# Optimization experiments

Measured on AMD Instinct MI355X. Metric: run time of the kernel, lower is better.

Reference implementation:

```python
import jax, jax.numpy as jnp
import numpy as np

SIGMA = 0.4            # gaussian geodesic kernel width (class default)
B, N_IN, N_OUT, C, K = 2, 163842, 40962, 128, 7  # icosphere rank 7 -> rank 6, valence-7 candidates


def setup_inputs() -> dict:
    key = jax.random.key(0)
    k_x, k_p, k_o, k_c, k_d = jax.random.split(key, 5)
    x = jax.random.normal(k_x, (B, N_IN, C), dtype=jnp.float32)
    parent_idx = jax.random.randint(k_p, (N_IN,), 0, N_OUT)
    omega = jax.random.uniform(k_o, (N_IN,), dtype=jnp.float32, minval=0.5, maxval=1.5)
    omega = omega / omega.mean()          # matches omega / omega.mean() in __init__
    cand_idx = jax.random.randint(k_c, (N_IN, K), 0, N_OUT)
    cand_mask = jnp.ones((N_IN, K), dtype=jnp.float32)
    delta = jax.random.uniform(k_d, (N_IN, K), dtype=jnp.float32, minval=0.0, maxval=0.5)
    return dict(x=x, omega=omega, delta=delta, cand_mask=cand_mask,
                parent_idx=parent_idx, cand_idx=cand_idx)


def reference(x, omega, delta, cand_mask, parent_idx, cand_idx):
    # --- AreaWeightedDownsample: weight, scatter-add to coarse nodes, normalize ---
    weighted = x * omega[None, :, None]                        # [B, N_in, C]
    down = jnp.zeros((x.shape[0], N_OUT, x.shape[2]), x.dtype)
    down = down.at[:, parent_idx].add(weighted)                # scatter_add over node dim
    denom = jnp.zeros((N_OUT,), x.dtype).at[parent_idx].add(omega)
    down = down / jnp.clip(denom, 1e-8)[None, :, None]         # [B, N_out, C]
    # --- GeodesicKernelUpsample: gather K coarse candidates, gaussian geodesic weights ---
    w = jnp.exp(-(delta * delta) / (2.0 * SIGMA * SIGMA)) * cand_mask   # [N_in, K]
    w = w / jnp.clip(w.sum(axis=-1, keepdims=True), 1e-8)
    gathered = down[:, cand_idx]                               # [B, N_in, K, C]
    return jnp.einsum('nk,bnkc->bnc', w, gathered)             # [B, N_in, C]
```

## Files before the change

kernel.cpp:

```cpp
#include <hip/hip_runtime.h>
#include <hip/hip_bf16.h>

#define B_SZ   2
#define N_IN   163842
#define N_OUT  40962
#define C_DIM  128
#define K_CAND 7
#define INV_2SIG2 3.125f

#define SCAN_T 1024
#define NBLK_SCAN ((N_OUT + SCAN_T - 1) / SCAN_T)

typedef float f32x4 __attribute__((ext_vector_type(4)));
typedef unsigned short u16x8 __attribute__((ext_vector_type(8)));

__device__ __forceinline__ float bf2f(unsigned short u) {
    return __uint_as_float((unsigned)u << 16);
}
__device__ __forceinline__ unsigned short f2bf(float f) {
    unsigned u = __float_as_uint(f);
    return (unsigned short)((u + 0x7fffu + ((u >> 16) & 1u)) >> 16);
}

__global__ __launch_bounds__(256) void count_kernel(
    const int* __restrict__ parent, int* __restrict__ count)
{
    int n = blockIdx.x * 256 + threadIdx.x;
    if (n < N_IN) atomicAdd(&count[parent[n]], 1);
}

__global__ __launch_bounds__(SCAN_T) void scan1_kernel(
    const int* __restrict__ count, int* __restrict__ offs, int* __restrict__ bsum)
{
    __shared__ int wsum[SCAN_T / 64];
    const int t    = threadIdx.x;
    const int lane = t & 63;
    const int wid  = t >> 6;
    const int j    = blockIdx.x * SCAN_T + t;
    const int c = (j < N_OUT) ? count[j] : 0;

    int v = c;
    #pragma unroll
    for (int off = 1; off < 64; off <<= 1) {
        int u = __shfl_up(v, off, 64);
        if (lane >= off) v += u;
    }
    if (lane == 63) wsum[wid] = v;
    __syncthreads();
    if (wid == 0 && lane < SCAN_T / 64) {
        int w = wsum[lane];
        #pragma unroll
        for (int off = 1; off < SCAN_T / 64; off <<= 1) {
            int u = __shfl_up(w, off, 64);
            if (lane >= off) w += u;
        }
        wsum[lane] = w;
    }
    __syncthreads();
    const int wbase = (wid == 0) ? 0 : wsum[wid - 1];
    if (j < N_OUT) offs[j] = wbase + v - c;
    if (t == 0) bsum[blockIdx.x] = wsum[SCAN_T / 64 - 1];
}

__global__ __launch_bounds__(64) void scan2_kernel(
    const int* __restrict__ bsum, int* __restrict__ bbase)
{
    const int lane = threadIdx.x;
    int s = (lane < NBLK_SCAN) ? bsum[lane] : 0;
    int v = s;
    #pragma unroll
    for (int off = 1; off < 64; off <<= 1) {
        int u = __shfl_up(v, off, 64);
        if (lane >= off) v += u;
    }
    if (lane < NBLK_SCAN) bbase[lane] = v - s;
}

__global__ __launch_bounds__(SCAN_T) void scan3_kernel(
    int* __restrict__ offs, const int* __restrict__ bbase)
{
    const int j = blockIdx.x * SCAN_T + threadIdx.x;
    if (j < N_OUT && blockIdx.x > 0) offs[j] += bbase[blockIdx.x];
}

__global__ __launch_bounds__(256) void fill_kernel(
    const int* __restrict__ parent, const int* __restrict__ offs,
    const float* __restrict__ omega,
    int* __restrict__ count, int* __restrict__ perm,
    float* __restrict__ om_perm)
{
    int n = blockIdx.x * 256 + threadIdx.x;
    if (n < N_IN) {
        const int p = parent[n];
        const float om = omega[n];
        const int pos = offs[p] + atomicSub(&count[p], 1) - 1;
        perm[pos] = n;
        om_perm[pos] = om;
    }
}

__global__ __launch_bounds__(256) void reduce_kernel(
    const float* __restrict__ x,
    const int*   __restrict__ offs,
    const int*   __restrict__ perm,
    const float* __restrict__ om_perm,
    __hip_bfloat16* __restrict__ down)
{
    const int wid  = threadIdx.x >> 6;
    const int lane = threadIdx.x & 63;
    const int p = blockIdx.x * 4 + wid;
    if (p >= N_OUT) return;

    const int beg = offs[p];
    const int end = (p + 1 < N_OUT) ? offs[p + 1] : N_IN;
    const int cnt = end - beg;

    const int half = lane >> 5;
    const int l    = lane & 31;
    const f32x4* x4 = (const f32x4*)x;
    const size_t bofs = (size_t)half * N_IN * 32;

    f32x4 acc = {0.f, 0.f, 0.f, 0.f};
    float ds = 0.f;

    for (int cbase = 0; cbase < cnt; cbase += 64) {
        const int m = min(64, cnt - cbase);
        int   myn  = 0;
        float myom = 0.f;
        if (lane < m) {
            myn  = perm[beg + cbase + lane];
            myom = om_perm[beg + cbase + lane];
        }
        #pragma unroll 4
        for (int j = 0; j < m; ++j) {
            const int   n  = __shfl(myn,  j);
            const float om = __shfl(myom, j);
            ds += om;
            const f32x4 v = __builtin_nontemporal_load(&x4[bofs + (size_t)n * 32 + l]);
            acc.x = fmaf(v.x, om, acc.x);
            acc.y = fmaf(v.y, om, acc.y);
            acc.z = fmaf(v.z, om, acc.z);
            acc.w = fmaf(v.w, om, acc.w);
        }
    }
    const float inv = 1.f / fmaxf(ds, 1e-8f);

    ushort4 hh;
    hh.x = f2bf(acc.x * inv);
    hh.y = f2bf(acc.y * inv);
    hh.z = f2bf(acc.z * inv);
    hh.w = f2bf(acc.w * inv);
    ((ushort4*)down)[((size_t)half * N_OUT + p) * 32 + l] = hh;
}

__global__ __launch_bounds__(256) void gather_kernel(
    const float* __restrict__ delta,
    const float* __restrict__ cand_mask,
    const int*   __restrict__ cand_idx,
    const __hip_bfloat16* __restrict__ down,
    float* __restrict__ out)
{
    const int wid  = threadIdx.x >> 6;
    const int lane = threadIdx.x & 63;
    const int grp  = lane >> 5;
    const int l5   = lane & 31;
    const int n0   = blockIdx.x * 16 + wid * 4 + grp * 2;
    if (n0 >= N_IN) return;
    const bool r1ok = (n0 + 1 < N_IN);

    const int sub = l5 >> 3;
    const int ls  = l5 & 7;
    float w = 0.f;
    int pidx = 0;
    if (sub < 2 && ls < K_CAND && (sub == 0 || r1ok)) {
        const int n = n0 + sub;
        const float d   = delta[(size_t)n * K_CAND + ls];
        const float msk = cand_mask[(size_t)n * K_CAND + ls];
        pidx = cand_idx[(size_t)n * K_CAND + ls];
        w = __expf(-d * d * INV_2SIG2) * msk;
    }
    float s = w;
    s += __shfl_xor(s, 1, 8);
    s += __shfl_xor(s, 2, 8);
    s += __shfl_xor(s, 4, 8);
    const float coef = w / fmaxf(s, 1e-8f);

    float cf[2][K_CAND];
    int   pk[2][K_CAND];
    #pragma unroll
    for (int r = 0; r < 2; ++r) {
        #pragma unroll
        for (int k = 0; k < K_CAND; ++k) {
            cf[r][k] = __shfl(coef, r * 8 + k, 32);
            pk[r][k] = __shfl(pidx, r * 8 + k, 32);
        }
    }

    const int half = l5 >> 4;
    const int l4   = l5 & 15;
    const u16x8* d8 = (const u16x8*)down;
    const size_t bofs = (size_t)half * N_OUT * 16;

    u16x8 v[2][K_CAND];
    #pragma unroll
    for (int r = 0; r < 2; ++r)
        #pragma unroll
        for (int k = 0; k < K_CAND; ++k)
            v[r][k] = d8[bofs + (size_t)pk[r][k] * 16 + l4];

    f32x4* o4 = (f32x4*)out;
    #pragma unroll
    for (int r = 0; r < 2; ++r) {
        f32x4 acc0 = {0.f, 0.f, 0.f, 0.f};
        f32x4 acc1 = {0.f, 0.f, 0.f, 0.f};
        #pragma unroll
        for (int k = 0; k < K_CAND; ++k) {
            const float c = cf[r][k];
            acc0.x = fmaf(c, bf2f(v[r][k].s0), acc0.x);
            acc0.y = fmaf(c, bf2f(v[r][k].s1), acc0.y);
            acc0.z = fmaf(c, bf2f(v[r][k].s2), acc0.z);
            acc0.w = fmaf(c, bf2f(v[r][k].s3), acc0.w);
            acc1.x = fmaf(c, bf2f(v[r][k].s4), acc1.x);
            acc1.y = fmaf(c, bf2f(v[r][k].s5), acc1.y);
            acc1.z = fmaf(c, bf2f(v[r][k].s6), acc1.z);
            acc1.w = fmaf(c, bf2f(v[r][k].s7), acc1.w);
        }
        if (r == 0 || r1ok) {
            const size_t obase = ((size_t)half * N_IN + n0 + r) * 32 + (size_t)l4 * 2;
            __builtin_nontemporal_store(acc0, &o4[obase]);
            __builtin_nontemporal_store(acc1, &o4[obase + 1]);
        }
    }
}

extern "C" void kernel_launch(void* const* d_in, const int* in_sizes, int n_in,
                              void* d_out, int out_size, void* d_ws, size_t ws_size,
                              hipStream_t stream) {
    const float* x         = (const float*)d_in[0];
    const float* omega     = (const float*)d_in[1];
    const float* delta     = (const float*)d_in[2];
    const float* cand_mask = (const float*)d_in[3];
    const int*   parent    = (const int*)d_in[4];
    const int*   cand_idx  = (const int*)d_in[5];
    float* out = (float*)d_out;

    __hip_bfloat16* down = (__hip_bfloat16*)d_ws;
    int*   count   = (int*)(down + (size_t)B_SZ * N_OUT * C_DIM);
    int*   offs    = count + N_OUT;
    int*   perm    = offs + N_OUT;
    float* om_perm = (float*)(perm + N_IN);
    int*   bsum    = (int*)(om_perm + N_IN);
    int*   bbase   = bsum + NBLK_SCAN;

    hipMemsetAsync(count, 0, (size_t)N_OUT * sizeof(int), stream);

    const int nblk = (N_IN + 255) / 256;
    count_kernel<<<nblk, 256, 0, stream>>>(parent, count);
    scan1_kernel<<<NBLK_SCAN, SCAN_T, 0, stream>>>(count, offs, bsum);
    scan2_kernel<<<1, 64, 0, stream>>>(bsum, bbase);
    scan3_kernel<<<NBLK_SCAN, SCAN_T, 0, stream>>>(offs, bbase);
    fill_kernel<<<nblk, 256, 0, stream>>>(parent, offs, omega, count, perm, om_perm);
    reduce_kernel<<<(N_OUT + 3) / 4, 256, 0, stream>>>(x, offs, perm, om_perm, down);
    gather_kernel<<<(N_IN + 15) / 16, 256, 0, stream>>>(
        delta, cand_mask, cand_idx, down, out);
}
```

Baseline: 397.1 us.

## Persistent grid-stride gather with metadata prefetch and interleaved batch layout for down

The gather kernel becomes persistent with a fixed grid. It prefetches the next pair's delta, mask and index loads while the current pair's candidate rows are gathered and accumulated. The down buffer is stored with both batches interleaved per coarse node, so each candidate fetch reads one contiguous 512-byte row instead of two separate rows. The reduce unroll and launch bounds are also raised. The intent is to hide index-load latency and improve gather locality, at the cost of higher register pressure and a fixed grid size.

```diff
diff --git a/kernel.cpp b/kernel.cpp
--- a/kernel.cpp
+++ b/kernel.cpp
@@ -10,6 +10,7 @@
 
 #define SCAN_T 1024
 #define NBLK_SCAN ((N_OUT + SCAN_T - 1) / SCAN_T)
+#define GATHER_BLOCKS 2048
 
 typedef float f32x4 __attribute__((ext_vector_type(4)));
 typedef unsigned short u16x8 __attribute__((ext_vector_type(8)));
@@ -99,7 +100,7 @@
     }
 }
 
-__global__ __launch_bounds__(256) void reduce_kernel(
+__global__ __launch_bounds__(256, 4) void reduce_kernel(
     const float* __restrict__ x,
     const int*   __restrict__ offs,
     const int*   __restrict__ perm,
@@ -131,7 +132,7 @@
             myn  = perm[beg + cbase + lane];
             myom = om_perm[beg + cbase + lane];
         }
-        #pragma unroll 4
+        #pragma unroll 8
         for (int j = 0; j < m; ++j) {
             const int   n  = __shfl(myn,  j);
             const float om = __shfl(myom, j);
@@ -150,10 +151,10 @@
     hh.y = f2bf(acc.y * inv);
     hh.z = f2bf(acc.z * inv);
     hh.w = f2bf(acc.w * inv);
-    ((ushort4*)down)[((size_t)half * N_OUT + p) * 32 + l] = hh;
-}
-
-__global__ __launch_bounds__(256) void gather_kernel(
+    ((ushort4*)down)[(size_t)p * 64 + lane] = hh;
+}
+
+__global__ __launch_bounds__(256, 4) void gather_kernel(
     const float* __restrict__ delta,
     const float* __restrict__ cand_mask,
     const int*   __restrict__ cand_idx,
@@ -164,72 +165,90 @@
     const int lane = threadIdx.x & 63;
     const int grp  = lane >> 5;
     const int l5   = lane & 31;
-    const int n0   = blockIdx.x * 16 + wid * 4 + grp * 2;
-    if (n0 >= N_IN) return;
-    const bool r1ok = (n0 + 1 < N_IN);
+    const int gid  = (blockIdx.x * 4 + wid) * 2 + grp;
+    const int ngroups = GATHER_BLOCKS * 8;
+    const int npairs  = N_IN / 2;
 
     const int sub = l5 >> 3;
     const int ls  = l5 & 7;
+
+    const u16x8* d8 = (const u16x8*)down;
+    f32x4* o4 = (f32x4*)out;
+    const int half = l5 >> 4;
+    const int c16  = l5 & 15;
+
     float w = 0.f;
     int pidx = 0;
-    if (sub < 2 && ls < K_CAND && (sub == 0 || r1ok)) {
-        const int n = n0 + sub;
-        const float d   = delta[(size_t)n * K_CAND + ls];
-        const float msk = cand_mask[(size_t)n * K_CAND + ls];
-        pidx = cand_idx[(size_t)n * K_CAND + ls];
-        w = __expf(-d * d * INV_2SIG2) * msk;
-    }
-    float s = w;
-    s += __shfl_xor(s, 1, 8);
-    s += __shfl_xor(s, 2, 8);
-    s += __shfl_xor(s, 4, 8);
-    const float coef = w / fmaxf(s, 1e-8f);
-
-    float cf[2][K_CAND];
-    int   pk[2][K_CAND];
-    #pragma unroll
-    for (int r = 0; r < 2; ++r) {
-        #pragma unroll
-        for (int k = 0; k < K_CAND; ++k) {
-            cf[r][k] = __shfl(coef, r * 8 + k, 32);
-            pk[r][k] = __shfl(pidx, r * 8 + k, 32);
-        }
-    }
-
-    const int half = l5 >> 4;
-    const int l4   = l5 & 15;
-    const u16x8* d8 = (const u16x8*)down;
-    const size_t bofs = (size_t)half * N_OUT * 16;
-
-    u16x8 v[2][K_CAND];
-    #pragma unroll
-    for (int r = 0; r < 2; ++r)
-        #pragma unroll
-        for (int k = 0; k < K_CAND; ++k)
-            v[r][k] = d8[bofs + (size_t)pk[r][k] * 16 + l4];
-
-    f32x4* o4 = (f32x4*)out;
-    #pragma unroll
-    for (int r = 0; r < 2; ++r) {
-        f32x4 acc0 = {0.f, 0.f, 0.f, 0.f};
-        f32x4 acc1 = {0.f, 0.f, 0.f, 0.f};
-        #pragma unroll
-        for (int k = 0; k < K_CAND; ++k) {
-            const float c = cf[r][k];
-            acc0.x = fmaf(c, bf2f(v[r][k].s0), acc0.x);
-            acc0.y = fmaf(c, bf2f(v[r][k].s1), acc0.y);
-            acc0.z = fmaf(c, bf2f(v[r][k].s2), acc0.z);
-            acc0.w = fmaf(c, bf2f(v[r][k].s3), acc0.w);
-            acc1.x = fmaf(c, bf2f(v[r][k].s4), acc1.x);
-            acc1.y = fmaf(c, bf2f(v[r][k].s5), acc1.y);
-            acc1.z = fmaf(c, bf2f(v[r][k].s6), acc1.z);
-            acc1.w = fmaf(c, bf2f(v[r][k].s7), acc1.w);
-        }
-        if (r == 0 || r1ok) {
-            const size_t obase = ((size_t)half * N_IN + n0 + r) * 32 + (size_t)l4 * 2;
+    {
+        const int pi = gid;
+        if (pi < npairs && sub < 2 && ls < K_CAND) {
+            const int n = pi * 2 + sub;
+            const float d   = __builtin_nontemporal_load(&delta[(size_t)n * K_CAND + ls]);
+            const float msk = __builtin_nontemporal_load(&cand_mask[(size_t)n * K_CAND + ls]);
+            pidx = __builtin_nontemporal_load(&cand_idx[(size_t)n * K_CAND + ls]);
+            w = __expf(-d * d * INV_2SIG2) * msk;
+        }
+    }
+
+    for (int pi = gid; pi < npairs; pi += ngroups) {
+        float s = w;
+        s += __shfl_xor(s, 1, 8);
+        s += __shfl_xor(s, 2, 8);
+        s += __shfl_xor(s, 4, 8);
+        const float coef = w / fmaxf(s, 1e-8f);
+
+        float cf[2][K_CAND];
+        int   pk[2][K_CAND];
+        #pragma unroll
+        for (int r = 0; r < 2; ++r)
+            #pragma unroll
+            for (int k = 0; k < K_CAND; ++k) {
+                cf[r][k] = __shfl(coef, r * 8 + k, 32);
+                pk[r][k] = __shfl(pidx, r * 8 + k, 32);
+            }
+
+        u16x8 v[2][K_CAND];
+        #pragma unroll
+        for (int r = 0; r < 2; ++r)
+            #pragma unroll
+            for (int k = 0; k < K_CAND; ++k)
+                v[r][k] = d8[(size_t)pk[r][k] * 32 + l5];
+
+        const int pn = pi + ngroups;
+        float w2 = 0.f;
+        int pidx2 = 0;
+        if (pn < npairs && sub < 2 && ls < K_CAND) {
+            const int n = pn * 2 + sub;
+            const float d   = __builtin_nontemporal_load(&delta[(size_t)n * K_CAND + ls]);
+            const float msk = __builtin_nontemporal_load(&cand_mask[(size_t)n * K_CAND + ls]);
+            pidx2 = __builtin_nontemporal_load(&cand_idx[(size_t)n * K_CAND + ls]);
+            w2 = __expf(-d * d * INV_2SIG2) * msk;
+        }
+
+        const int n0 = pi * 2;
+        #pragma unroll
+        for (int r = 0; r < 2; ++r) {
+            f32x4 acc0 = {0.f, 0.f, 0.f, 0.f};
+            f32x4 acc1 = {0.f, 0.f, 0.f, 0.f};
+            #pragma unroll
+            for (int k = 0; k < K_CAND; ++k) {
+                const float c = cf[r][k];
+                acc0.x = fmaf(c, bf2f(v[r][k].s0), acc0.x);
+                acc0.y = fmaf(c, bf2f(v[r][k].s1), acc0.y);
+                acc0.z = fmaf(c, bf2f(v[r][k].s2), acc0.z);
+                acc0.w = fmaf(c, bf2f(v[r][k].s3), acc0.w);
+                acc1.x = fmaf(c, bf2f(v[r][k].s4), acc1.x);
+                acc1.y = fmaf(c, bf2f(v[r][k].s5), acc1.y);
+                acc1.z = fmaf(c, bf2f(v[r][k].s6), acc1.z);
+                acc1.w = fmaf(c, bf2f(v[r][k].s7), acc1.w);
+            }
+            const size_t obase = ((size_t)half * N_IN + n0 + r) * 32 + (size_t)c16 * 2;
             __builtin_nontemporal_store(acc0, &o4[obase]);
             __builtin_nontemporal_store(acc1, &o4[obase + 1]);
         }
+
+        w = w2;
+        pidx = pidx2;
     }
 }
 
@@ -261,6 +280,6 @@
     scan3_kernel<<<NBLK_SCAN, SCAN_T, 0, stream>>>(offs, bbase);
     fill_kernel<<<nblk, 256, 0, stream>>>(parent, offs, omega, count, perm, om_perm);
     reduce_kernel<<<(N_OUT + 3) / 4, 256, 0, stream>>>(x, offs, perm, om_perm, down);
-    gather_kernel<<<(N_IN + 15) / 16, 256, 0, stream>>>(
+    gather_kernel<<<GATHER_BLOCKS, 256, 0, stream>>>(
         delta, cand_mask, cand_idx, down, out);
 }
```

After: 404.1 us. Within noise of the previous version (+1.8%).

## Interleave batch dimension in bf16 coarse buffer so each gather reads contiguous 256B rows

Applied to the files above, without the earlier changes.

The coarse bf16 buffer moves from [B][N_out][C] to [N_out][B][C], so both batch rows of a coarse node sit next to each other. The reduce kernel now has each half-wave handle one coarse node for both batches, and the gather kernel has each half-wave handle one fine node and fetch one contiguous 512B row per candidate. The aim is to halve the index and weight loads per batch and improve locality of the random gather. In exchange each lane issues fewer independent loads per thread in the gather (7 instead of 14), which may reduce memory-level parallelism.

```diff
diff --git a/kernel.cpp b/kernel.cpp
--- a/kernel.cpp
+++ b/kernel.cpp
@@ -108,49 +108,55 @@
 {
     const int wid  = threadIdx.x >> 6;
     const int lane = threadIdx.x & 63;
-    const int p = blockIdx.x * 4 + wid;
+    const int grp  = lane >> 5;
+    const int l5   = lane & 31;
+    const int p = blockIdx.x * 8 + wid * 2 + grp;
     if (p >= N_OUT) return;
 
     const int beg = offs[p];
     const int end = (p + 1 < N_OUT) ? offs[p + 1] : N_IN;
     const int cnt = end - beg;
 
-    const int half = lane >> 5;
-    const int l    = lane & 31;
     const f32x4* x4 = (const f32x4*)x;
-    const size_t bofs = (size_t)half * N_IN * 32;
-
-    f32x4 acc = {0.f, 0.f, 0.f, 0.f};
+
+    f32x4 acc0 = {0.f, 0.f, 0.f, 0.f};
+    f32x4 acc1 = {0.f, 0.f, 0.f, 0.f};
     float ds = 0.f;
 
-    for (int cbase = 0; cbase < cnt; cbase += 64) {
-        const int m = min(64, cnt - cbase);
+    for (int cbase = 0; cbase < cnt; cbase += 32) {
+        const int m = min(32, cnt - cbase);
         int   myn  = 0;
         float myom = 0.f;
-        if (lane < m) {
-            myn  = perm[beg + cbase + lane];
-            myom = om_perm[beg + cbase + lane];
+        if (l5 < m) {
+            myn  = perm[beg + cbase + l5];
+            myom = om_perm[beg + cbase + l5];
         }
         #pragma unroll 4
         for (int j = 0; j < m; ++j) {
-            const int   n  = __shfl(myn,  j);
-            const float om = __shfl(myom, j);
+            const int   n  = __shfl(myn,  j, 32);
+            const float om = __shfl(myom, j, 32);
             ds += om;
-            const f32x4 v = __builtin_nontemporal_load(&x4[bofs + (size_t)n * 32 + l]);
-            acc.x = fmaf(v.x, om, acc.x);
-            acc.y = fmaf(v.y, om, acc.y);
-            acc.z = fmaf(v.z, om, acc.z);
-            acc.w = fmaf(v.w, om, acc.w);
+            const f32x4 v0 = __builtin_nontemporal_load(&x4[(size_t)n * 32 + l5]);
+            const f32x4 v1 = __builtin_nontemporal_load(&x4[((size_t)N_IN + n) * 32 + l5]);
+            acc0.x = fmaf(v0.x, om, acc0.x);
+            acc0.y = fmaf(v0.y, om, acc0.y);
+            acc0.z = fmaf(v0.z, om, acc0.z);
+            acc0.w = fmaf(v0.w, om, acc0.w);
+            acc1.x = fmaf(v1.x, om, acc1.x);
+            acc1.y = fmaf(v1.y, om, acc1.y);
+            acc1.z = fmaf(v1.z, om, acc1.z);
+            acc1.w = fmaf(v1.w, om, acc1.w);
         }
     }
     const float inv = 1.f / fmaxf(ds, 1e-8f);
 
-    ushort4 hh;
-    hh.x = f2bf(acc.x * inv);
-    hh.y = f2bf(acc.y * inv);
-    hh.z = f2bf(acc.z * inv);
-    hh.w = f2bf(acc.w * inv);
-    ((ushort4*)down)[((size_t)half * N_OUT + p) * 32 + l] = hh;
+    ushort4 h0, h1;
+    h0.x = f2bf(acc0.x * inv); h0.y = f2bf(acc0.y * inv);
+    h0.z = f2bf(acc0.z * inv); h0.w = f2bf(acc0.w * inv);
+    h1.x = f2bf(acc1.x * inv); h1.y = f2bf(acc1.y * inv);
+    h1.z = f2bf(acc1.z * inv); h1.w = f2bf(acc1.w * inv);
+    ((ushort4*)down)[(size_t)p * 64 + l5]      = h0;
+    ((ushort4*)down)[(size_t)p * 64 + 32 + l5] = h1;
 }
 
 __global__ __launch_bounds__(256) void gather_kernel(
@@ -164,19 +170,15 @@
     const int lane = threadIdx.x & 63;
     const int grp  = lane >> 5;
     const int l5   = lane & 31;
-    const int n0   = blockIdx.x * 16 + wid * 4 + grp * 2;
-    if (n0 >= N_IN) return;
-    const bool r1ok = (n0 + 1 < N_IN);
-
-    const int sub = l5 >> 3;
-    const int ls  = l5 & 7;
+    const int n    = blockIdx.x * 8 + wid * 2 + grp;
+    if (n >= N_IN) return;
+
     float w = 0.f;
     int pidx = 0;
-    if (sub < 2 && ls < K_CAND && (sub == 0 || r1ok)) {
-        const int n = n0 + sub;
-        const float d   = delta[(size_t)n * K_CAND + ls];
-        const float msk = cand_mask[(size_t)n * K_CAND + ls];
-        pidx = cand_idx[(size_t)n * K_CAND + ls];
+    if (l5 < K_CAND) {
+        const float d   = __builtin_nontemporal_load(&delta[(size_t)n * K_CAND + l5]);
+        const float msk = __builtin_nontemporal_load(&cand_mask[(size_t)n * K_CAND + l5]);
+        pidx = __builtin_nontemporal_load(&cand_idx[(size_t)n * K_CAND + l5]);
         w = __expf(-d * d * INV_2SIG2) * msk;
     }
     float s = w;
@@ -185,52 +187,40 @@
     s += __shfl_xor(s, 4, 8);
     const float coef = w / fmaxf(s, 1e-8f);
 
-    float cf[2][K_CAND];
-    int   pk[2][K_CAND];
-    #pragma unroll
-    for (int r = 0; r < 2; ++r) {
-        #pragma unroll
-        for (int k = 0; k < K_CAND; ++k) {
-            cf[r][k] = __shfl(coef, r * 8 + k, 32);
-            pk[r][k] = __shfl(pidx, r * 8 + k, 32);
-        }
-    }
-
+    float cf[K_CAND];
+    int   pk[K_CAND];
+    #pragma unroll
+    for (int k = 0; k < K_CAND; ++k) {
+        cf[k] = __shfl(coef, k, 32);
+        pk[k] = __shfl(pidx, k, 32);
+    }
+
+    const u16x8* d8 = (const u16x8*)down;
+    u16x8 v[K_CAND];
+    #pragma unroll
+    for (int k = 0; k < K_CAND; ++k)
+        v[k] = d8[(size_t)pk[k] * 32 + l5];
+
+    f32x4 acc0 = {0.f, 0.f, 0.f, 0.f};
+    f32x4 acc1 = {0.f, 0.f, 0.f, 0.f};
+    #pragma unroll
+    for (int k = 0; k < K_CAND; ++k) {
+        const float c = cf[k];
+        acc0.x = fmaf(c, bf2f(v[k].s0), acc0.x);
+        acc0.y = fmaf(c, bf2f(v[k].s1), acc0.y);
+        acc0.z = fmaf(c, bf2f(v[k].s2), acc0.z);
+        acc0.w = fmaf(c, bf2f(v[k].s3), acc0.w);
+        acc1.x = fmaf(c, bf2f(v[k].s4), acc1.x);
+        acc1.y = fmaf(c, bf2f(v[k].s5), acc1.y);
+        acc1.z = fmaf(c, bf2f(v[k].s6), acc1.z);
+        acc1.w = fmaf(c, bf2f(v[k].s7), acc1.w);
+    }
     const int half = l5 >> 4;
-    const int l4   = l5 & 15;
-    const u16x8* d8 = (const u16x8*)down;
-    const size_t bofs = (size_t)half * N_OUT * 16;
-
-    u16x8 v[2][K_CAND];
-    #pragma unroll
-    for (int r = 0; r < 2; ++r)
-        #pragma unroll
-        for (int k = 0; k < K_CAND; ++k)
-            v[r][k] = d8[bofs + (size_t)pk[r][k] * 16 + l4];
-
+    const int c8   = l5 & 15;
     f32x4* o4 = (f32x4*)out;
-    #pragma unroll
-    for (int r = 0; r < 2; ++r) {
-        f32x4 acc0 = {0.f, 0.f, 0.f, 0.f};
-        f32x4 acc1 = {0.f, 0.f, 0.f, 0.f};
-        #pragma unroll
-        for (int k = 0; k < K_CAND; ++k) {
-            const float c = cf[r][k];
-            acc0.x = fmaf(c, bf2f(v[r][k].s0), acc0.x);
-            acc0.y = fmaf(c, bf2f(v[r][k].s1), acc0.y);
-            acc0.z = fmaf(c, bf2f(v[r][k].s2), acc0.z);
-            acc0.w = fmaf(c, bf2f(v[r][k].s3), acc0.w);
-            acc1.x = fmaf(c, bf2f(v[r][k].s4), acc1.x);
-            acc1.y = fmaf(c, bf2f(v[r][k].s5), acc1.y);
-            acc1.z = fmaf(c, bf2f(v[r][k].s6), acc1.z);
-            acc1.w = fmaf(c, bf2f(v[r][k].s7), acc1.w);
-        }
-        if (r == 0 || r1ok) {
-            const size_t obase = ((size_t)half * N_IN + n0 + r) * 32 + (size_t)l4 * 2;
-            __builtin_nontemporal_store(acc0, &o4[obase]);
-            __builtin_nontemporal_store(acc1, &o4[obase + 1]);
-        }
-    }
+    const size_t obase = ((size_t)half * N_IN + n) * 32 + (size_t)c8 * 2;
+    __builtin_nontemporal_store(acc0, &o4[obase]);
+    __builtin_nontemporal_store(acc1, &o4[obase + 1]);
 }
 
 extern "C" void kernel_launch(void* const* d_in, const int* in_sizes, int n_in,
@@ -260,7 +250,7 @@
     scan2_kernel<<<1, 64, 0, stream>>>(bsum, bbase);
     scan3_kernel<<<NBLK_SCAN, SCAN_T, 0, stream>>>(offs, bbase);
     fill_kernel<<<nblk, 256, 0, stream>>>(parent, offs, omega, count, perm, om_perm);
-    reduce_kernel<<<(N_OUT + 3) / 4, 256, 0, stream>>>(x, offs, perm, om_perm, down);
-    gather_kernel<<<(N_IN + 15) / 16, 256, 0, stream>>>(
+    reduce_kernel<<<(N_OUT + 7) / 8, 256, 0, stream>>>(x, offs, perm, om_perm, down);
+    gather_kernel<<<(N_IN + 7) / 8, 256, 0, stream>>>(
         delta, cand_mask, cand_idx, down, out);
 }
```

Result: no change. 396.9 us (-0.1%).
